# Optimization experiments

Measured on AMD Instinct MI355X. Metric: run time of the kernel, lower is better.

## Reference

```python
import jax, jax.numpy as jnp
import numpy as np

B, N, F_IN, F_OUT, H = 8, 1024, 256, 256, 4
HD = F_OUT // H  # head_dim = 64
NEG_SLOPE = 0.2


def setup_inputs() -> dict:
    key = jax.random.key(0)
    k1, k2, k3 = jax.random.split(key, 3)
    x = jax.random.normal(k1, (B, N, F_IN), dtype=jnp.float32)
    adj = jnp.ones((B, N, N), dtype=jnp.int32)
    # Linear weight, stored as [in, out] so h = x @ W
    W = jax.random.normal(k2, (F_IN, F_OUT), dtype=jnp.float32) / np.sqrt(F_IN)
    # attention vector a: [H, 2*head_dim], xavier-ish init
    a = jax.random.normal(k3, (H, 2 * HD), dtype=jnp.float32) * np.sqrt(2.0 / (H + 2 * HD))
    return {"x": x, "adj": adj, "W": W, "a": a}


def reference(x, adj, W, a):
    Bq, Nq, _ = x.shape
    h = (x @ W).reshape(Bq, Nq, H, HD).transpose(0, 2, 1, 3)  # [B,H,N,HD]
    a1, a2 = a[:, :HD], a[:, HD:]  # decompose concat: e_nm = h_n.a1 + h_m.a2
    s1 = jnp.einsum('bhnd,hd->bhn', h, a1)
    s2 = jnp.einsum('bhmd,hd->bhm', h, a2)
    e = jax.nn.leaky_relu(s1[:, :, :, None] + s2[:, :, None, :], NEG_SLOPE)  # [B,H,N,N]
    e = jnp.where(adj[:, None, :, :] == 0, -jnp.inf, e)
    attention = jax.nn.softmax(e, axis=-1)
    out = jnp.einsum('bhnm,bhmd->bhnd', attention, h)
    return out.transpose(0, 2, 1, 3).reshape(Bq, Nq, H * HD)
```

## Files before the change

kernel.cpp:

```cpp
#include <hip/hip_runtime.h>
#include <math.h>

#define H 4
#define HD 64
#define NN 1024
#define BB 8
#define FIN 256
#define FOUT 256

typedef _Float16 f16x8 __attribute__((ext_vector_type(8)));
typedef _Float16 f16x4 __attribute__((ext_vector_type(4)));
typedef float f32x4 __attribute__((ext_vector_type(4)));

__global__ __launch_bounds__(256) void gemm_xw(const float* __restrict__ x,
                                               const float* __restrict__ W,
                                               const float* __restrict__ a,
                                               _Float16* __restrict__ hT,
                                               float* __restrict__ s1_ws,
                                               float* __restrict__ s2_ws) {
  __shared__ _Float16 xs[64][72];
  __shared__ _Float16 wst[64][72];
  const int tid = threadIdx.x;
  const int lane = tid & 63, w = tid >> 6;
  const int c = lane & 15, q = lane >> 4;
  const int bn0 = blockIdx.x * 64;
  const int head = blockIdx.y;
  const int b = bn0 >> 10;
  const int nb = bn0 & 1023;
  const int bh = b * H + head;

  f32x4 acc[4];
#pragma unroll
  for (int t = 0; t < 4; ++t) acc[t] = (f32x4){0.f, 0.f, 0.f, 0.f};

  const int srow = tid >> 2;
  const int skoff = (tid & 3) * 16;

  for (int ch = 0; ch < 4; ++ch) {
    {
      const float* xp = x + (size_t)(bn0 + srow) * FIN + ch * 64 + skoff;
      f16x8 v0, v1;
#pragma unroll
      for (int i = 0; i < 8; ++i) v0[i] = (_Float16)xp[i];
#pragma unroll
      for (int i = 0; i < 8; ++i) v1[i] = (_Float16)xp[8 + i];
      *(f16x8*)&xs[srow][skoff] = v0;
      *(f16x8*)&xs[srow][skoff + 8] = v1;
    }
    {
      const float* wp = W + (size_t)(ch * 64 + lane) * FOUT + head * 64 + w * 16;
#pragma unroll
      for (int i = 0; i < 16; ++i) wst[w * 16 + i][lane] = (_Float16)wp[i];
    }
    __syncthreads();
#pragma unroll
    for (int ks = 0; ks < 2; ++ks) {
      f16x8 af = *(const f16x8*)&xs[w * 16 + c][ks * 32 + q * 8];
#pragma unroll
      for (int t = 0; t < 4; ++t) {
        f16x8 bf = *(const f16x8*)&wst[t * 16 + c][ks * 32 + q * 8];
        acc[t] = __builtin_amdgcn_mfma_f32_16x16x32_f16(af, bf, acc[t], 0, 0, 0);
      }
    }
    __syncthreads();
  }

  float a1v[4], a2v[4];
#pragma unroll
  for (int t = 0; t < 4; ++t) {
    a1v[t] = a[head * 2 * HD + t * 16 + c];
    a2v[t] = a[head * 2 * HD + HD + t * 16 + c];
  }
  float s1p[4] = {0.f, 0.f, 0.f, 0.f};
  float s2p[4] = {0.f, 0.f, 0.f, 0.f};
#pragma unroll
  for (int t = 0; t < 4; ++t) {
    f16x4 hv;
#pragma unroll
    for (int rr = 0; rr < 4; ++rr) {
      hv[rr] = (_Float16)acc[t][rr];
      s1p[rr] += acc[t][rr] * a1v[t];
      s2p[rr] += acc[t][rr] * a2v[t];
    }
    *(f16x4*)&hT[((size_t)(bh * 64 + t * 16 + c)) * NN + nb + w * 16 + q * 4] = hv;
  }
#pragma unroll
  for (int rr = 0; rr < 4; ++rr) {
    float s1 = s1p[rr], s2 = s2p[rr];
#pragma unroll
    for (int off = 8; off; off >>= 1) {
      s1 += __shfl_xor(s1, off);
      s2 += __shfl_xor(s2, off);
    }
    if (c == 0) {
      int n = nb + w * 16 + q * 4 + rr;
      s1_ws[(size_t)bh * NN + n] = s1;
      s2_ws[(size_t)bh * NN + n] = s2;
    }
  }
}

__global__ __launch_bounds__(256) void attn(const _Float16* __restrict__ hT,
                                            const float* __restrict__ s1_ws,
                                            const float* __restrict__ s2_ws,
                                            const int* __restrict__ adj,
                                            float* __restrict__ out) {
  __shared__ float s2_all[NN];
  __shared__ float s1_blk[64];
  __shared__ unsigned short mskT[64][64];
  __shared__ _Float16 pt[2][64][88];
  __shared__ float L_lds[64];
  const int tid = threadIdx.x, lane = tid & 63, w = tid >> 6;
  const int c = lane & 15, q = lane >> 4;
  const int ntile = blockIdx.x, bh = blockIdx.y;
  const int b = bh >> 2, head = bh & 3;
  const int n0 = ntile * 64;

  {
    float4 v = *(const float4*)&s2_ws[(size_t)bh * NN + tid * 4];
    *(float4*)&s2_all[tid * 4] = v;
    if (tid < 64) s1_blk[tid] = s1_ws[(size_t)bh * NN + n0 + tid];
  }
  __syncthreads();

  float S1[16];
#pragma unroll
  for (int r = 0; r < 16; ++r) S1[r] = s1_blk[w * 16 + r];

  float M[16];
#pragma unroll
  for (int r = 0; r < 16; ++r) M[r] = -1e30f;
  const int* adjp = adj + ((size_t)(b * NN + n0 + w * 16)) * NN + lane;
  for (int ch = 0; ch < 16; ++ch) {
    int av[16];
#pragma unroll
    for (int r = 0; r < 16; ++r) av[r] = adjp[(size_t)r * NN + ch * 64];
    float s2v = s2_all[ch * 64 + lane];
    unsigned bits = 0;
#pragma unroll
    for (int r = 0; r < 16; ++r) {
      float e = S1[r] + s2v;
      e = fmaxf(e, 0.2f * e);
      bits |= (av[r] != 0) ? (1u << r) : 0u;
      e = (av[r] != 0) ? e : -1e30f;
      M[r] = fmaxf(M[r], e);
    }
    mskT[w * 16 + ch][lane] = (unsigned short)bits;
  }
#pragma unroll
  for (int r = 0; r < 16; ++r) {
    float m = M[r];
#pragma unroll
    for (int off = 32; off; off >>= 1) m = fmaxf(m, __shfl_xor(m, off));
    M[r] = m;
  }

  float Lp[16];
#pragma unroll
  for (int r = 0; r < 16; ++r) Lp[r] = 0.f;
  f32x4 acc[4];
#pragma unroll
  for (int t = 0; t < 4; ++t) acc[t] = (f32x4){0.f, 0.f, 0.f, 0.f};
  const _Float16* bptr = hT + (size_t)bh * 64 * NN + (size_t)(w * 16 + c) * NN + q * 8;

  for (int ch = 0; ch < 16; ++ch) {
    const int m0 = ch * 64;
    const int buf = ch & 1;
    float s2v = s2_all[m0 + lane];
    unsigned mbits = mskT[w * 16 + ch][lane];
#pragma unroll
    for (int r = 0; r < 16; ++r) {
      float e = S1[r] + s2v;
      e = fmaxf(e, 0.2f * e);
      e = ((mbits >> r) & 1) ? e : -1e30f;
      float p = __expf(e - M[r]);
      Lp[r] += p;
      pt[buf][w * 16 + r][lane] = (_Float16)p;
    }
    f16x8 bf0 = *(const f16x8*)(bptr + m0);
    f16x8 bf1 = *(const f16x8*)(bptr + m0 + 32);
    __syncthreads();
#pragma unroll
    for (int t = 0; t < 4; ++t) {
      f16x8 af0 = *(const f16x8*)&pt[buf][t * 16 + c][q * 8];
      f16x8 af1 = *(const f16x8*)&pt[buf][t * 16 + c][32 + q * 8];
      acc[t] = __builtin_amdgcn_mfma_f32_16x16x32_f16(af0, bf0, acc[t], 0, 0, 0);
      acc[t] = __builtin_amdgcn_mfma_f32_16x16x32_f16(af1, bf1, acc[t], 0, 0, 0);
    }
  }

  float lv = 0.f;
#pragma unroll
  for (int r = 0; r < 16; ++r) {
    float s = Lp[r];
#pragma unroll
    for (int off = 32; off; off >>= 1) s += __shfl_xor(s, off);
    lv = (lane == r) ? s : lv;
  }
  if (lane < 16) L_lds[w * 16 + lane] = lv;
  __syncthreads();
#pragma unroll
  for (int t = 0; t < 4; ++t) {
#pragma unroll
    for (int rr = 0; rr < 4; ++rr) {
      int nloc = t * 16 + q * 4 + rr;
      out[((size_t)(b * NN + n0 + nloc)) * FOUT + head * 64 + w * 16 + c] =
          acc[t][rr] / L_lds[nloc];
    }
  }
}

extern "C" void kernel_launch(void* const* d_in, const int* in_sizes, int n_in,
                              void* d_out, int out_size, void* d_ws, size_t ws_size,
                              hipStream_t stream) {
  const float* x = (const float*)d_in[0];
  const int* adj = (const int*)d_in[1];
  const float* W = (const float*)d_in[2];
  const float* a = (const float*)d_in[3];
  float* out = (float*)d_out;

  _Float16* hT = (_Float16*)d_ws;
  float* s1_ws = (float*)((char*)d_ws + (size_t)BB * H * HD * NN * sizeof(_Float16));
  float* s2_ws = s1_ws + (size_t)BB * H * NN;

  gemm_xw<<<dim3(128, 4), 256, 0, stream>>>(x, W, a, hT, s1_ws, s2_ws);
  attn<<<dim3(16, 32), 256, 0, stream>>>(hT, s1_ws, s2_ws, adj, out);
}
```

Measured before the change: 120.9 us.

## Factor softmax exponentials per row/column, pre-transpose W, halve attention row tile

Adds a kernel that transposes W to fp16 once, so the GEMM reads it directly instead of converting it with strided loads. The GEMM now stages all of x in LDS and precomputes exp(s2) and exp(0.2*s2) per column. The attention kernel rewrites exp(leaky(s1+s2)-M) as a product of per-row and per-column exponentials chosen by sign, which removes the per-element expf. It also uses 32-row tiles for more blocks, int2 adjacency loads, and 128-wide chunks. The factored form risks overflow or underflow when s values are large, and it adds a third launch.

After: 125.3 us. 1.04x slower.

```diff
diff --git a/kernel.cpp b/kernel.cpp
--- a/kernel.cpp
+++ b/kernel.cpp
@@ -10,59 +10,72 @@
 
 typedef _Float16 f16x8 __attribute__((ext_vector_type(8)));
 typedef _Float16 f16x4 __attribute__((ext_vector_type(4)));
+typedef _Float16 f16x2 __attribute__((ext_vector_type(2)));
 typedef float f32x4 __attribute__((ext_vector_type(4)));
 
+__global__ __launch_bounds__(256) void wtrans(const float* __restrict__ W,
+                                              _Float16* __restrict__ WT) {
+  __shared__ float tile[64][68];
+  const int tid = threadIdx.x;
+  const int k0 = (blockIdx.x & 3) * 64, f0 = (blockIdx.x >> 2) * 64;
+  const int r = tid >> 4, c4 = (tid & 15) * 4;
+#pragma unroll
+  for (int p = 0; p < 4; ++p) {
+    float4 v = *(const float4*)&W[(size_t)(k0 + p * 16 + r) * FOUT + f0 + c4];
+    *(float4*)&tile[p * 16 + r][c4] = v;
+  }
+  __syncthreads();
+  const int f = tid >> 2, kg = (tid & 3) * 16;
+#pragma unroll
+  for (int i = 0; i < 4; ++i) {
+    f16x4 o;
+#pragma unroll
+    for (int j = 0; j < 4; ++j) o[j] = (_Float16)tile[kg + i * 4 + j][f];
+    *(f16x4*)&WT[(size_t)(f0 + f) * FIN + k0 + kg + i * 4] = o;
+  }
+}
+
 __global__ __launch_bounds__(256) void gemm_xw(const float* __restrict__ x,
-                                               const float* __restrict__ W,
+                                               const _Float16* __restrict__ WT,
                                                const float* __restrict__ a,
                                                _Float16* __restrict__ hT,
                                                float* __restrict__ s1_ws,
-                                               float* __restrict__ s2_ws) {
-  __shared__ _Float16 xs[64][72];
-  __shared__ _Float16 wst[64][72];
+                                               float* __restrict__ s2_ws,
+                                               float* __restrict__ u_ws,
+                                               float* __restrict__ v_ws) {
+  __shared__ _Float16 xs[64][264];
   const int tid = threadIdx.x;
   const int lane = tid & 63, w = tid >> 6;
   const int c = lane & 15, q = lane >> 4;
   const int bn0 = blockIdx.x * 64;
   const int head = blockIdx.y;
-  const int b = bn0 >> 10;
-  const int nb = bn0 & 1023;
+  const int b = bn0 >> 10, nb = bn0 & 1023;
   const int bh = b * H + head;
 
+#pragma unroll
+  for (int p = 0; p < 16; ++p) {
+    int f = p * 256 + tid;
+    int row = f >> 6, col = (f & 63) * 4;
+    float4 v = *(const float4*)&x[(size_t)(bn0 + row) * FIN + col];
+    f16x4 h4;
+    h4[0] = (_Float16)v.x; h4[1] = (_Float16)v.y;
+    h4[2] = (_Float16)v.z; h4[3] = (_Float16)v.w;
+    *(f16x4*)&xs[row][col] = h4;
+  }
+  __syncthreads();
+
   f32x4 acc[4];
 #pragma unroll
   for (int t = 0; t < 4; ++t) acc[t] = (f32x4){0.f, 0.f, 0.f, 0.f};
-
-  const int srow = tid >> 2;
-  const int skoff = (tid & 3) * 16;
-
-  for (int ch = 0; ch < 4; ++ch) {
-    {
-      const float* xp = x + (size_t)(bn0 + srow) * FIN + ch * 64 + skoff;
-      f16x8 v0, v1;
-#pragma unroll
-      for (int i = 0; i < 8; ++i) v0[i] = (_Float16)xp[i];
-#pragma unroll
-      for (int i = 0; i < 8; ++i) v1[i] = (_Float16)xp[8 + i];
-      *(f16x8*)&xs[srow][skoff] = v0;
-      *(f16x8*)&xs[srow][skoff + 8] = v1;
-    }
-    {
-      const float* wp = W + (size_t)(ch * 64 + lane) * FOUT + head * 64 + w * 16;
-#pragma unroll
-      for (int i = 0; i < 16; ++i) wst[w * 16 + i][lane] = (_Float16)wp[i];
-    }
-    __syncthreads();
-#pragma unroll
-    for (int ks = 0; ks < 2; ++ks) {
-      f16x8 af = *(const f16x8*)&xs[w * 16 + c][ks * 32 + q * 8];
-#pragma unroll
-      for (int t = 0; t < 4; ++t) {
-        f16x8 bf = *(const f16x8*)&wst[t * 16 + c][ks * 32 + q * 8];
-        acc[t] = __builtin_amdgcn_mfma_f32_16x16x32_f16(af, bf, acc[t], 0, 0, 0);
-      }
-    }
-    __syncthreads();
+  const _Float16* wbase = WT + (size_t)head * 64 * FIN;
+#pragma unroll
+  for (int ks = 0; ks < 8; ++ks) {
+    f16x8 af = *(const f16x8*)&xs[w * 16 + c][ks * 32 + q * 8];
+#pragma unroll
+    for (int t = 0; t < 4; ++t) {
+      f16x8 bf = *(const f16x8*)&wbase[(size_t)(t * 16 + c) * FIN + ks * 32 + q * 8];
+      acc[t] = __builtin_amdgcn_mfma_f32_16x16x32_f16(af, bf, acc[t], 0, 0, 0);
+    }
   }
 
   float a1v[4], a2v[4];
@@ -94,8 +107,11 @@
     }
     if (c == 0) {
       int n = nb + w * 16 + q * 4 + rr;
-      s1_ws[(size_t)bh * NN + n] = s1;
-      s2_ws[(size_t)bh * NN + n] = s2;
+      size_t idx = (size_t)bh * NN + n;
+      s1_ws[idx] = s1;
+      s2_ws[idx] = s2;
+      u_ws[idx] = __expf(s2);
+      v_ws[idx] = __expf(0.2f * s2);
     }
   }
 }
@@ -103,109 +119,123 @@
 __global__ __launch_bounds__(256) void attn(const _Float16* __restrict__ hT,
                                             const float* __restrict__ s1_ws,
                                             const float* __restrict__ s2_ws,
+                                            const float* __restrict__ u_ws,
+                                            const float* __restrict__ v_ws,
                                             const int* __restrict__ adj,
                                             float* __restrict__ out) {
-  __shared__ float s2_all[NN];
-  __shared__ float s1_blk[64];
-  __shared__ unsigned short mskT[64][64];
-  __shared__ _Float16 pt[2][64][88];
-  __shared__ float L_lds[64];
+  __shared__ float s2r[NN], uu[NN], vv[NN];
+  __shared__ _Float16 pt[2][32][136];
+  __shared__ float invL[32];
   const int tid = threadIdx.x, lane = tid & 63, w = tid >> 6;
   const int c = lane & 15, q = lane >> 4;
   const int ntile = blockIdx.x, bh = blockIdx.y;
   const int b = bh >> 2, head = bh & 3;
-  const int n0 = ntile * 64;
+  const int n0 = ntile * 32;
 
   {
-    float4 v = *(const float4*)&s2_ws[(size_t)bh * NN + tid * 4];
-    *(float4*)&s2_all[tid * 4] = v;
-    if (tid < 64) s1_blk[tid] = s1_ws[(size_t)bh * NN + n0 + tid];
-  }
-  __syncthreads();
-
-  float S1[16];
-#pragma unroll
-  for (int r = 0; r < 16; ++r) S1[r] = s1_blk[w * 16 + r];
-
-  float M[16];
-#pragma unroll
-  for (int r = 0; r < 16; ++r) M[r] = -1e30f;
-  const int* adjp = adj + ((size_t)(b * NN + n0 + w * 16)) * NN + lane;
-  for (int ch = 0; ch < 16; ++ch) {
-    int av[16];
-#pragma unroll
-    for (int r = 0; r < 16; ++r) av[r] = adjp[(size_t)r * NN + ch * 64];
-    float s2v = s2_all[ch * 64 + lane];
-    unsigned bits = 0;
-#pragma unroll
-    for (int r = 0; r < 16; ++r) {
-      float e = S1[r] + s2v;
-      e = fmaxf(e, 0.2f * e);
-      bits |= (av[r] != 0) ? (1u << r) : 0u;
-      e = (av[r] != 0) ? e : -1e30f;
-      M[r] = fmaxf(M[r], e);
-    }
-    mskT[w * 16 + ch][lane] = (unsigned short)bits;
-  }
-#pragma unroll
-  for (int r = 0; r < 16; ++r) {
-    float m = M[r];
+    size_t base = (size_t)bh * NN + tid * 4;
+    *(float4*)&s2r[tid * 4] = *(const float4*)&s2_ws[base];
+    *(float4*)&uu[tid * 4] = *(const float4*)&u_ws[base];
+    *(float4*)&vv[tid * 4] = *(const float4*)&v_ws[base];
+  }
+  __syncthreads();
+
+  float s1v[8];
+#pragma unroll
+  for (int r = 0; r < 8; ++r) s1v[r] = s1_ws[(size_t)bh * NN + n0 + w * 8 + r];
+
+  float mx[8];
+  unsigned msk[8];
+#pragma unroll
+  for (int r = 0; r < 8; ++r) { mx[r] = -INFINITY; msk[r] = 0u; }
+  const int* adjp = adj + ((size_t)(b * NN + n0 + w * 8)) * NN + 2 * lane;
+#pragma unroll
+  for (int ch = 0; ch < 8; ++ch) {
+    int2 av[8];
+#pragma unroll
+    for (int r = 0; r < 8; ++r) av[r] = *(const int2*)(adjp + (size_t)r * NN + ch * 128);
+    float2 s2p = *(const float2*)&s2r[ch * 128 + 2 * lane];
+#pragma unroll
+    for (int r = 0; r < 8; ++r) {
+      bool e0 = av[r].x != 0, e1 = av[r].y != 0;
+      msk[r] |= (e0 ? (1u << (2 * ch)) : 0u) | (e1 ? (2u << (2 * ch)) : 0u);
+      mx[r] = fmaxf(mx[r], e0 ? s2p.x : -INFINITY);
+      mx[r] = fmaxf(mx[r], e1 ? s2p.y : -INFINITY);
+    }
+  }
+  float Arow[8], Brow[8], ns1[8];
+#pragma unroll
+  for (int r = 0; r < 8; ++r) {
+    float m = mx[r];
 #pragma unroll
     for (int off = 32; off; off >>= 1) m = fmaxf(m, __shfl_xor(m, off));
-    M[r] = m;
-  }
-
-  float Lp[16];
-#pragma unroll
-  for (int r = 0; r < 16; ++r) Lp[r] = 0.f;
-  f32x4 acc[4];
-#pragma unroll
-  for (int t = 0; t < 4; ++t) acc[t] = (f32x4){0.f, 0.f, 0.f, 0.f};
-  const _Float16* bptr = hT + (size_t)bh * 64 * NN + (size_t)(w * 16 + c) * NN + q * 8;
-
-  for (int ch = 0; ch < 16; ++ch) {
-    const int m0 = ch * 64;
+    float t0 = s1v[r] + m;
+    float M = fmaxf(t0, 0.2f * t0);
+    Arow[r] = __expf(s1v[r] - M);
+    Brow[r] = __expf(0.2f * s1v[r] - M);
+    ns1[r] = -s1v[r];
+  }
+
+  float Lp[8];
+#pragma unroll
+  for (int r = 0; r < 8; ++r) Lp[r] = 0.f;
+  f32x4 acc[2];
+  acc[0] = (f32x4){0.f, 0.f, 0.f, 0.f};
+  acc[1] = (f32x4){0.f, 0.f, 0.f, 0.f};
+  const _Float16* bptr = hT + ((size_t)bh * 64 + w * 16 + c) * NN + q * 8;
+
+  for (int ch = 0; ch < 8; ++ch) {
     const int buf = ch & 1;
-    float s2v = s2_all[m0 + lane];
-    unsigned mbits = mskT[w * 16 + ch][lane];
-#pragma unroll
-    for (int r = 0; r < 16; ++r) {
-      float e = S1[r] + s2v;
-      e = fmaxf(e, 0.2f * e);
-      e = ((mbits >> r) & 1) ? e : -1e30f;
-      float p = __expf(e - M[r]);
-      Lp[r] += p;
-      pt[buf][w * 16 + r][lane] = (_Float16)p;
-    }
-    f16x8 bf0 = *(const f16x8*)(bptr + m0);
-    f16x8 bf1 = *(const f16x8*)(bptr + m0 + 32);
+    f16x8 bf0 = *(const f16x8*)(bptr + ch * 128);
+    f16x8 bf1 = *(const f16x8*)(bptr + ch * 128 + 32);
+    f16x8 bf2 = *(const f16x8*)(bptr + ch * 128 + 64);
+    f16x8 bf3 = *(const f16x8*)(bptr + ch * 128 + 96);
+    float2 s2p = *(const float2*)&s2r[ch * 128 + 2 * lane];
+    float2 up = *(const float2*)&uu[ch * 128 + 2 * lane];
+    float2 vp = *(const float2*)&vv[ch * 128 + 2 * lane];
+#pragma unroll
+    for (int r = 0; r < 8; ++r) {
+      bool m0 = (msk[r] >> (2 * ch)) & 1u;
+      bool m1 = (msk[r] >> (2 * ch + 1)) & 1u;
+      float p0 = (s2p.x >= ns1[r]) ? Arow[r] * up.x : Brow[r] * vp.x;
+      float p1 = (s2p.y >= ns1[r]) ? Arow[r] * up.y : Brow[r] * vp.y;
+      p0 = m0 ? p0 : 0.f;
+      p1 = m1 ? p1 : 0.f;
+      Lp[r] += p0 + p1;
+      f16x2 pk = __builtin_bit_cast(f16x2, __builtin_amdgcn_cvt_pkrtz(p0, p1));
+      *(f16x2*)&pt[buf][w * 8 + r][2 * lane] = pk;
+    }
     __syncthreads();
 #pragma unroll
-    for (int t = 0; t < 4; ++t) {
-      f16x8 af0 = *(const f16x8*)&pt[buf][t * 16 + c][q * 8];
-      f16x8 af1 = *(const f16x8*)&pt[buf][t * 16 + c][32 + q * 8];
-      acc[t] = __builtin_amdgcn_mfma_f32_16x16x32_f16(af0, bf0, acc[t], 0, 0, 0);
-      acc[t] = __builtin_amdgcn_mfma_f32_16x16x32_f16(af1, bf1, acc[t], 0, 0, 0);
-    }
-  }
-
-  float lv = 0.f;
-#pragma unroll
-  for (int r = 0; r < 16; ++r) {
+    for (int t = 0; t < 2; ++t) {
+      f16x8 a0 = *(const f16x8*)&pt[buf][t * 16 + c][q * 8];
+      f16x8 a1 = *(const f16x8*)&pt[buf][t * 16 + c][32 + q * 8];
+      f16x8 a2 = *(const f16x8*)&pt[buf][t * 16 + c][64 + q * 8];
+      f16x8 a3 = *(const f16x8*)&pt[buf][t * 16 + c][96 + q * 8];
+      acc[t] = __builtin_amdgcn_mfma_f32_16x16x32_f16(a0, bf0, acc[t], 0, 0, 0);
+      acc[t] = __builtin_amdgcn_mfma_f32_16x16x32_f16(a1, bf1, acc[t], 0, 0, 0);
+      acc[t] = __builtin_amdgcn_mfma_f32_16x16x32_f16(a2, bf2, acc[t], 0, 0, 0);
+      acc[t] = __builtin_amdgcn_mfma_f32_16x16x32_f16(a3, bf3, acc[t], 0, 0, 0);
+    }
+  }
+
+  float myL = 0.f;
+#pragma unroll
+  for (int r = 0; r < 8; ++r) {
     float s = Lp[r];
 #pragma unroll
     for (int off = 32; off; off >>= 1) s += __shfl_xor(s, off);
-    lv = (lane == r) ? s : lv;
-  }
-  if (lane < 16) L_lds[w * 16 + lane] = lv;
-  __syncthreads();
-#pragma unroll
-  for (int t = 0; t < 4; ++t) {
+    if (lane == r) myL = s;
+  }
+  if (lane < 8) invL[w * 8 + lane] = 1.0f / myL;
+  __syncthreads();
+#pragma unroll
+  for (int t = 0; t < 2; ++t) {
 #pragma unroll
     for (int rr = 0; rr < 4; ++rr) {
       int nloc = t * 16 + q * 4 + rr;
       out[((size_t)(b * NN + n0 + nloc)) * FOUT + head * 64 + w * 16 + c] =
-          acc[t][rr] / L_lds[nloc];
+          acc[t][rr] * invL[nloc];
     }
   }
 }
@@ -219,10 +249,15 @@
   const float* a = (const float*)d_in[3];
   float* out = (float*)d_out;
 
-  _Float16* hT = (_Float16*)d_ws;
-  float* s1_ws = (float*)((char*)d_ws + (size_t)BB * H * HD * NN * sizeof(_Float16));
+  char* ws = (char*)d_ws;
+  _Float16* hT = (_Float16*)ws;
+  _Float16* WT = (_Float16*)(ws + (size_t)4 * 1024 * 1024);
+  float* s1_ws = (float*)(ws + (size_t)4 * 1024 * 1024 + 128 * 1024);
   float* s2_ws = s1_ws + (size_t)BB * H * NN;
-
-  gemm_xw<<<dim3(128, 4), 256, 0, stream>>>(x, W, a, hT, s1_ws, s2_ws);
-  attn<<<dim3(16, 32), 256, 0, stream>>>(hT, s1_ws, s2_ws, adj, out);
-}
+  float* u_ws = s2_ws + (size_t)BB * H * NN;
+  float* v_ws = u_ws + (size_t)BB * H * NN;
+
+  wtrans<<<16, 256, 0, stream>>>(W, WT);
+  gemm_xw<<<dim3(128, 4), 256, 0, stream>>>(x, WT, a, hT, s1_ws, s2_ws, u_ws, v_ws);
+  attn<<<dim3(32, 32), 256, 0, stream>>>(hT, s1_ws, s2_ws, u_ws, v_ws, adj, out);
+}
```
